# Kernel tuning notes

Hardware: AMD Instinct MI355X
Metric: run time of the kernel (lower is better)

The kernel has to match this reference:

```python
import jax, jax.numpy as jnp
import numpy as np

B, LQ, LK = 4, 1024, 2048
DQ, DK, DV, D = 1024, 512, 512, 1024
H = 16
HD = D // H
EPS = 1e-5


def setup_inputs() -> dict:
    key = jax.random.key(0)
    ks = jax.random.split(key, 12)
    s = lambda fan: 1.0 / np.sqrt(fan)
    return {
        "query": jax.random.normal(ks[0], (B, LQ, DQ), jnp.float32),
        "key": jax.random.normal(ks[1], (B, LK, DK), jnp.float32),
        "value": jax.random.normal(ks[2], (B, LK, DV), jnp.float32),
        "key_padding_mask": jnp.ones((B, LK), jnp.int32),
        "Wq": jax.random.normal(ks[3], (DQ, D), jnp.float32) * s(DQ),
        "bq": jnp.zeros((D,), jnp.float32),
        "Wk": jax.random.normal(ks[4], (DK, D), jnp.float32) * s(DK),
        "bk": jnp.zeros((D,), jnp.float32),
        "Wv": jax.random.normal(ks[5], (DV, D), jnp.float32) * s(DV),
        "bv": jnp.zeros((D,), jnp.float32),
        "Wo": jax.random.normal(ks[6], (D, D), jnp.float32) * s(D),
        "bo": jnp.zeros((D,), jnp.float32),
        "ln_g": jnp.ones((D,), jnp.float32),
        "ln_b": jnp.zeros((D,), jnp.float32),
    }


def _layer_norm(x, g, b):
    mu = jnp.mean(x, axis=-1, keepdims=True)
    var = jnp.mean(jnp.square(x - mu), axis=-1, keepdims=True)
    return (x - mu) * jax.lax.rsqrt(var + EPS) * g + b


def reference(query, key, value, key_padding_mask, Wq, bq, Wk, bk, Wv, bv, Wo, bo, ln_g, ln_b):
    residual = query
    qn = _layer_norm(query, ln_g, ln_b)
    # projections -> [B, L, H, HD]
    q = (qn @ Wq + bq).reshape(B, LQ, H, HD)
    k = (key @ Wk + bk).reshape(B, LK, H, HD)
    v = (value @ Wv + bv).reshape(B, LK, H, HD)
    scale = HD ** -0.5
    # scores [B, H, Lq, Lk]
    scores = jnp.einsum("bqhd,bkhd->bhqk", q, k) * scale
    mask = (key_padding_mask != 0)[:, None, None, :]  # True = keep
    scores = jnp.where(mask, scores, -jnp.inf)
    attn = jax.nn.softmax(scores, axis=-1)
    # dropout is identity in eval mode
    ctx = jnp.einsum("bhqk,bkhd->bqhd", attn, v).reshape(B, LQ, D)
    out = ctx @ Wo + bo
    return out + residual
```

## Files before the change

### kernel.cpp

```cpp
#include <hip/hip_runtime.h>
#include <hip/hip_bf16.h>
#include <stdint.h>

#define Bn 4
#define LQ 1024
#define LK 2048
#define Dm 1024
#define Hn 16
#define HD 64

typedef __attribute__((ext_vector_type(4))) float f32x4;
typedef __attribute__((ext_vector_type(8))) short bf16x8;
typedef __attribute__((ext_vector_type(2))) uint32_t u32x2;

__device__ __forceinline__ ushort f2bf(float f) {
  union { float f; uint32_t u; } v; v.f = f;
  uint32_t r = v.u + 0x7FFF + ((v.u >> 16) & 1);
  return (ushort)(r >> 16);
}

__device__ __forceinline__ uint32_t cvt_pk_bf16(float lo, float hi) {
  uint32_t r;
  asm("v_cvt_pk_bf16_f32 %0, %1, %2" : "=v"(r) : "v"(lo), "v"(hi));
  return r;
}

__device__ __forceinline__ float exp2v(float x) {
  float r;
  asm("v_exp_f32 %0, %1" : "=v"(r) : "v"(x));
  return r;
}

__device__ __forceinline__ void gload16(const void* g, void* lds) {
  __builtin_amdgcn_global_load_lds(
      (const __attribute__((address_space(1))) void*)g,
      (__attribute__((address_space(3))) void*)lds, 16, 0, 0);
}

__device__ __forceinline__ void wait_vm0_barrier() {
  asm volatile("s_waitcnt vmcnt(0)" ::: "memory");
  __builtin_amdgcn_s_barrier();
}

__global__ __launch_bounds__(256) void transpose_cast_kernel(
    const float* __restrict__ W, ushort* __restrict__ Wt, int K, int N) {
  __shared__ float tile[64][65];
  int k0 = blockIdx.x * 64, n0 = blockIdx.y * 64;
  int tx = threadIdx.x & 63, ty = threadIdx.x >> 6;
#pragma unroll
  for (int i = 0; i < 16; ++i) {
    int r = ty + i * 4;
    tile[r][tx] = W[(size_t)(k0 + r) * N + n0 + tx];
  }
  __syncthreads();
#pragma unroll
  for (int i = 0; i < 16; ++i) {
    int r = ty + i * 4;
    Wt[(size_t)(n0 + r) * K + k0 + tx] = f2bf(tile[tx][r]);
  }
}

__global__ __launch_bounds__(256) void cast_bf16_kernel(
    const float4* __restrict__ in, ushort4* __restrict__ out, int n4) {
  int i = blockIdx.x * blockDim.x + threadIdx.x;
  int stride = gridDim.x * blockDim.x;
  for (; i < n4; i += stride) {
    float4 v = in[i];
    out[i] = make_ushort4(f2bf(v.x), f2bf(v.y), f2bf(v.z), f2bf(v.w));
  }
}

__global__ __launch_bounds__(256) void ln_kernel(
    const float* __restrict__ x, const float* __restrict__ g,
    const float* __restrict__ b, ushort* __restrict__ y) {
  int row = blockIdx.x;
  const float4* xr = (const float4*)(x + (size_t)row * 1024);
  float4 v = xr[threadIdx.x];
  float s1 = v.x + v.y + v.z + v.w;
  float s2 = v.x * v.x + v.y * v.y + v.z * v.z + v.w * v.w;
#pragma unroll
  for (int off = 32; off > 0; off >>= 1) {
    s1 += __shfl_down(s1, off);
    s2 += __shfl_down(s2, off);
  }
  __shared__ float r1[4], r2[4];
  int w = threadIdx.x >> 6, lane = threadIdx.x & 63;
  if (lane == 0) { r1[w] = s1; r2[w] = s2; }
  __syncthreads();
  s1 = r1[0] + r1[1] + r1[2] + r1[3];
  s2 = r2[0] + r2[1] + r2[2] + r2[3];
  float mu = s1 * (1.0f / 1024.0f);
  float var = s2 * (1.0f / 1024.0f) - mu * mu;
  float rstd = rsqrtf(var + 1e-5f);
  float4 gv = ((const float4*)g)[threadIdx.x];
  float4 bv = ((const float4*)b)[threadIdx.x];
  ushort4 o;
  o.x = f2bf((v.x - mu) * rstd * gv.x + bv.x);
  o.y = f2bf((v.y - mu) * rstd * gv.y + bv.y);
  o.z = f2bf((v.z - mu) * rstd * gv.z + bv.z);
  o.w = f2bf((v.w - mu) * rstd * gv.w + bv.w);
  ((ushort4*)(y + (size_t)row * 1024))[threadIdx.x] = o;
}

template <int EPI>
__global__ __launch_bounds__(512) void gemm_bt_kernel(
    const ushort* __restrict__ A, const ushort* __restrict__ Bt,
    const float* __restrict__ bias, void* __restrict__ Cout,
    const float* __restrict__ residual, int M, int N, int K, float osc) {
  __shared__ ushort As[2][128 * 64];
  __shared__ ushort Bs[2][128 * 64];
  const int t = threadIdx.x;
  const int lane = t & 63;
  const int w = t >> 6;
  const int wm = w >> 2, wn = w & 3;
  const int m0 = blockIdx.y * 128, n0 = blockIdx.x * 128;
  const int l15 = lane & 15, g = lane >> 4;

  f32x4 acc[4][2] = {};

  const int c0 = t, c1 = t + 512;
  const int r0 = c0 >> 3, x0 = ((c0 & 7) ^ (r0 & 7)) * 8;
  const int r1 = c1 >> 3, x1 = ((c1 & 7) ^ (r1 & 7)) * 8;
  const ushort* Ap0 = A + (size_t)(m0 + r0) * K + x0;
  const ushort* Ap1 = A + (size_t)(m0 + r1) * K + x1;
  const ushort* Bp0 = Bt + (size_t)(n0 + r0) * K + x0;
  const ushort* Bp1 = Bt + (size_t)(n0 + r1) * K + x1;

  auto stage = [&](int buf, int kt) {
    gload16(Ap0 + kt, (char*)As[buf] + c0 * 16);
    gload16(Ap1 + kt, (char*)As[buf] + c1 * 16);
    gload16(Bp0 + kt, (char*)Bs[buf] + c0 * 16);
    gload16(Bp1 + kt, (char*)Bs[buf] + c1 * 16);
  };

  stage(0, 0);
  wait_vm0_barrier();

  int cur = 0;
  for (int kt = 0; kt < K; kt += 64) {
    if (kt + 64 < K) stage(cur ^ 1, kt + 64);
    bf16x8 af[4][2], bfr[2][2];
#pragma unroll
    for (int m = 0; m < 4; ++m) {
      int row = wm * 64 + m * 16 + l15;
#pragma unroll
      for (int kc = 0; kc < 2; ++kc)
        af[m][kc] = *(const bf16x8*)(As[cur] + row * 64 + ((kc * 4 + g) ^ (row & 7)) * 8);
    }
#pragma unroll
    for (int n = 0; n < 2; ++n) {
      int row = wn * 32 + n * 16 + l15;
#pragma unroll
      for (int kc = 0; kc < 2; ++kc)
        bfr[n][kc] = *(const bf16x8*)(Bs[cur] + row * 64 + ((kc * 4 + g) ^ (row & 7)) * 8);
    }
#pragma unroll
    for (int m = 0; m < 4; ++m)
#pragma unroll
      for (int n = 0; n < 2; ++n)
#pragma unroll
        for (int kc = 0; kc < 2; ++kc)
          acc[m][n] = __builtin_amdgcn_mfma_f32_16x16x32_bf16(af[m][kc], bfr[n][kc], acc[m][n], 0, 0, 0);
    wait_vm0_barrier();
    cur ^= 1;
  }

  float bias_v[2];
#pragma unroll
  for (int n = 0; n < 2; ++n) bias_v[n] = bias[n0 + wn * 32 + n * 16 + l15];

#pragma unroll
  for (int m = 0; m < 4; ++m) {
#pragma unroll
    for (int n = 0; n < 2; ++n) {
      int col = n0 + wn * 32 + n * 16 + l15;
      if (EPI == 1) {
        int row_base = m0 + wm * 64 + m * 16 + g * 4;
        int bb = row_base >> 11;
        int key = row_base & 2047;
        int h = col >> 6, hd = col & 63;
        ushort4 pk;
        pk.x = f2bf(acc[m][n][0] + bias_v[n]);
        pk.y = f2bf(acc[m][n][1] + bias_v[n]);
        pk.z = f2bf(acc[m][n][2] + bias_v[n]);
        pk.w = f2bf(acc[m][n][3] + bias_v[n]);
        *(ushort4*)((ushort*)Cout + ((size_t)((bb * 16 + h) * 64 + hd)) * 2048 + key) = pk;
      } else {
#pragma unroll
        for (int j = 0; j < 4; ++j) {
          int row = m0 + wm * 64 + m * 16 + g * 4 + j;
          if (EPI == 0) {
            float v = (acc[m][n][j] + bias_v[n]) * osc;
            ((ushort*)Cout)[(size_t)row * N + col] = f2bf(v);
          } else {
            size_t idx = (size_t)row * N + col;
            ((float*)Cout)[idx] = acc[m][n][j] + bias_v[n] + residual[idx];
          }
        }
      }
    }
  }
}

__global__ __launch_bounds__(512) void attn_kernel(
    const ushort* __restrict__ Qb, const ushort* __restrict__ Kb,
    const ushort* __restrict__ Vt, const int* __restrict__ mask,
    ushort* __restrict__ ctx) {
  __shared__ float mbias[2048];
  __shared__ ushort Ks[2][64 * 64];
  __shared__ ushort Vs[2][64 * 64];
  __shared__ ushort Ps[8][16 * 64];

  const int t = threadIdx.x, lane = t & 63, w = t >> 6;
  const int l15 = lane & 15, g = lane >> 4, g4 = g * 4;
  int o = blockIdx.x;
  int logical = (o & 7) * 64 + (o >> 3);
  const int b = logical >> 7;
  const int h = (logical >> 3) & 15;
  const int q0 = (logical & 7) * 128;
  const int* maskp = mask + b * 2048;

  const int rA = t >> 3;
  const int xA = ((t & 7) ^ (rA & 7)) * 8;
  const ushort* kp = Kb + ((size_t)(b * 2048 + rA)) * 1024 + h * 64 + xA;
  const ushort* vp = Vt + ((size_t)((b * 16 + h) * 64 + rA)) * 2048 + xA;

  auto stageKV = [&](int buf) {
    gload16(kp, (char*)Ks[buf] + t * 16);
    gload16(vp, (char*)Vs[buf] + t * 16);
  };

  stageKV(0);
  for (int i = t; i < 2048; i += 512) mbias[i] = maskp[i] ? 0.0f : -1e30f;

  bf16x8 aq[2];
  {
    int qrow = q0 + w * 16 + l15;
    const ushort* qp = Qb + ((size_t)(b * 1024 + qrow)) * 1024 + h * 64;
    aq[0] = *(const bf16x8*)(qp + g * 8);
    aq[1] = *(const bf16x8*)(qp + 32 + g * 8);
  }

  f32x4 o_acc[4] = {};
  float m_run = -1e30f, l_run = 0.0f;

  wait_vm0_barrier();

  char* pw = (char*)Ps[w];
  const int swz = (l15 & 7) << 4;

  int cur = 0;
  for (int kt = 0; kt < 2048; kt += 64) {
    kp += 64 * 1024;
    vp += 64;
    if (kt + 64 < 2048) stageKV(cur ^ 1);

    f32x4 sacc[4] = {};
    __builtin_amdgcn_s_setprio(1);
#pragma unroll
    for (int n = 0; n < 4; ++n) {
      int key = n * 16 + l15;
#pragma unroll
      for (int kc = 0; kc < 2; ++kc) {
        int kb2 = (kc * 32 + g * 8) * 2;
        bf16x8 kf = *(const bf16x8*)((char*)Ks[cur] + key * 128 + (kb2 ^ ((key & 7) << 4)));
        sacc[n] = __builtin_amdgcn_mfma_f32_16x16x32_bf16(kf, aq[kc], sacc[n], 0, 0, 0);
      }
    }
    __builtin_amdgcn_s_setprio(0);

    float sv[4][4];
    float tm = -1e30f;
#pragma unroll
    for (int n = 0; n < 4; ++n) {
      float4 mb = *(const float4*)&mbias[kt + n * 16 + g4];
      sv[n][0] = sacc[n][0] + mb.x;
      sv[n][1] = sacc[n][1] + mb.y;
      sv[n][2] = sacc[n][2] + mb.z;
      sv[n][3] = sacc[n][3] + mb.w;
      tm = fmaxf(tm, fmaxf(fmaxf(sv[n][0], sv[n][1]), fmaxf(sv[n][2], sv[n][3])));
    }
    tm = fmaxf(tm, __shfl_xor(tm, 16));
    tm = fmaxf(tm, __shfl_xor(tm, 32));

    if (__any(tm - m_run > 11.5f)) {
      float mn = fmaxf(m_run, tm);
      float al = exp2v(m_run - mn);
      m_run = mn;
      l_run *= al;
      float ao[4];
#pragma unroll
      for (int j = 0; j < 4; ++j) ao[j] = __shfl(al, g4 + j);
#pragma unroll
      for (int df = 0; df < 4; ++df)
#pragma unroll
        for (int j = 0; j < 4; ++j) o_acc[df][j] *= ao[j];
    }

    float psum = 0.0f;
    u32x2 pk[4];
#pragma unroll
    for (int n = 0; n < 4; ++n) {
      float p0 = exp2v(sv[n][0] - m_run);
      float p1 = exp2v(sv[n][1] - m_run);
      float p2 = exp2v(sv[n][2] - m_run);
      float p3 = exp2v(sv[n][3] - m_run);
      psum += (p0 + p1) + (p2 + p3);
      pk[n][0] = cvt_pk_bf16(p0, p1);
      pk[n][1] = cvt_pk_bf16(p2, p3);
    }
    psum += __shfl_xor(psum, 16);
    psum += __shfl_xor(psum, 32);
    l_run += psum;

    char* prow = pw + l15 * 128;
#pragma unroll
    for (int n = 0; n < 4; ++n)
      *(u32x2*)(prow + ((n * 32 + g * 8) ^ swz)) = pk[n];

    __builtin_amdgcn_s_setprio(1);
#pragma unroll
    for (int kc = 0; kc < 2; ++kc) {
      int kb2 = (kc * 32 + g * 8) * 2;
      bf16x8 pa = *(const bf16x8*)(prow + ((kc * 64 + g * 16) ^ swz));
#pragma unroll
      for (int df = 0; df < 4; ++df) {
        int d = df * 16 + l15;
        bf16x8 bv = *(const bf16x8*)((char*)Vs[cur] + d * 128 + (kb2 ^ ((d & 7) << 4)));
        o_acc[df] = __builtin_amdgcn_mfma_f32_16x16x32_bf16(pa, bv, o_acc[df], 0, 0, 0);
      }
    }
    __builtin_amdgcn_s_setprio(0);

    wait_vm0_barrier();
    cur ^= 1;
  }

  float inv[4];
#pragma unroll
  for (int j = 0; j < 4; ++j) inv[j] = 1.0f / __shfl(l_run, g4 + j);
  int qrow_base = q0 + w * 16 + g4;
#pragma unroll
  for (int df = 0; df < 4; ++df) {
    int col = h * 64 + df * 16 + l15;
#pragma unroll
    for (int j = 0; j < 4; ++j) {
      int qrow = qrow_base + j;
      ctx[((size_t)(b * 1024 + qrow)) * 1024 + col] = f2bf(o_acc[df][j] * inv[j]);
    }
  }
}

extern "C" void kernel_launch(void* const* d_in, const int* in_sizes, int n_in,
                              void* d_out, int out_size, void* d_ws, size_t ws_size,
                              hipStream_t stream) {
  const float* query = (const float*)d_in[0];
  const float* key   = (const float*)d_in[1];
  const float* value = (const float*)d_in[2];
  const int*   mask  = (const int*)d_in[3];
  const float* Wq = (const float*)d_in[4];
  const float* bq = (const float*)d_in[5];
  const float* Wk = (const float*)d_in[6];
  const float* bk = (const float*)d_in[7];
  const float* Wv = (const float*)d_in[8];
  const float* bv = (const float*)d_in[9];
  const float* Wo = (const float*)d_in[10];
  const float* bo = (const float*)d_in[11];
  const float* ln_g = (const float*)d_in[12];
  const float* ln_b = (const float*)d_in[13];
  float* out = (float*)d_out;

  char* p = (char*)d_ws;
  auto alloc = [&](size_t elems) { ushort* r = (ushort*)p; p += elems * 2; return r; };
  ushort* WqT  = alloc((size_t)1024 * 1024);
  ushort* WkT  = alloc((size_t)1024 * 512);
  ushort* WvT  = alloc((size_t)1024 * 512);
  ushort* WoT  = alloc((size_t)1024 * 1024);
  ushort* qn   = alloc((size_t)4096 * 1024);
  ushort* keyb = alloc((size_t)8192 * 512);
  ushort* valb = alloc((size_t)8192 * 512);
  ushort* Qb   = alloc((size_t)4096 * 1024);
  ushort* Kb   = alloc((size_t)8192 * 1024);
  ushort* Vt   = alloc((size_t)8192 * 1024);
  ushort* ctx  = alloc((size_t)4096 * 1024);
  (void)ws_size; (void)in_sizes; (void)n_in; (void)out_size;

  const float QSCALE = 0.125f * 1.44269504f;

  dim3 blk(256);
  dim3 blk5(512);
  transpose_cast_kernel<<<dim3(16, 16), blk, 0, stream>>>(Wq, WqT, 1024, 1024);
  transpose_cast_kernel<<<dim3(8, 16),  blk, 0, stream>>>(Wk, WkT, 512, 1024);
  transpose_cast_kernel<<<dim3(8, 16),  blk, 0, stream>>>(Wv, WvT, 512, 1024);
  transpose_cast_kernel<<<dim3(16, 16), blk, 0, stream>>>(Wo, WoT, 1024, 1024);
  cast_bf16_kernel<<<dim3(1024), blk, 0, stream>>>((const float4*)key,   (ushort4*)keyb, (8192 * 512) / 4);
  cast_bf16_kernel<<<dim3(1024), blk, 0, stream>>>((const float4*)value, (ushort4*)valb, (8192 * 512) / 4);
  ln_kernel<<<dim3(4096), blk, 0, stream>>>(query, ln_g, ln_b, qn);

  gemm_bt_kernel<0><<<dim3(8, 32), blk5, 0, stream>>>(qn,   WqT, bq, Qb, nullptr, 4096, 1024, 1024, QSCALE);
  gemm_bt_kernel<0><<<dim3(8, 64), blk5, 0, stream>>>(keyb, WkT, bk, Kb, nullptr, 8192, 1024, 512, 1.0f);
  gemm_bt_kernel<1><<<dim3(8, 64), blk5, 0, stream>>>(valb, WvT, bv, Vt, nullptr, 8192, 1024, 512, 1.0f);

  attn_kernel<<<dim3(512), blk5, 0, stream>>>(Qb, Kb, Vt, mask, ctx);

  gemm_bt_kernel<2><<<dim3(8, 32), blk5, 0, stream>>>(ctx, WoT, bo, out, query, 4096, 1024, 1024, 1.0f);
}
```

Measured before the change: 163.3 us.

## Switch GEMM and attention to 32x32x16 MFMA with 4-wave blocks

Both the projection GEMMs and the attention kernel move from 16x16x32 to 32x32x16 bf16 MFMA tiles, with 256-thread blocks where each wave owns a 64x64 GEMM tile or 32 query rows. In attention, the P matrix now stays in registers and is rearranged with cross-half lane shuffles instead of going through an LDS round trip. The output is staged through LDS so ctx is written with 16-byte coalesced stores. The aim is fewer LDS reads per MFMA and less LDS traffic, at the cost of more accumulator registers per wave and fewer waves per block to hide latency.

```diff
diff --git a/kernel.cpp b/kernel.cpp
--- a/kernel.cpp
+++ b/kernel.cpp
@@ -10,8 +10,8 @@
 #define HD 64
 
 typedef __attribute__((ext_vector_type(4))) float f32x4;
+typedef __attribute__((ext_vector_type(16))) float f32x16;
 typedef __attribute__((ext_vector_type(8))) short bf16x8;
-typedef __attribute__((ext_vector_type(2))) uint32_t u32x2;
 
 __device__ __forceinline__ ushort f2bf(float f) {
   union { float f; uint32_t u; } v; v.f = f;
@@ -39,6 +39,11 @@
 
 __device__ __forceinline__ void wait_vm0_barrier() {
   asm volatile("s_waitcnt vmcnt(0)" ::: "memory");
+  __builtin_amdgcn_s_barrier();
+}
+
+__device__ __forceinline__ void wait_all_barrier() {
+  asm volatile("s_waitcnt vmcnt(0) lgkmcnt(0)" ::: "memory");
   __builtin_amdgcn_s_barrier();
 }
 
@@ -103,7 +108,7 @@
 }
 
 template <int EPI>
-__global__ __launch_bounds__(512) void gemm_bt_kernel(
+__global__ __launch_bounds__(256) void gemm_bt_kernel(
     const ushort* __restrict__ A, const ushort* __restrict__ Bt,
     const float* __restrict__ bias, void* __restrict__ Cout,
     const float* __restrict__ residual, int M, int N, int K, float osc) {
@@ -112,25 +117,28 @@
   const int t = threadIdx.x;
   const int lane = t & 63;
   const int w = t >> 6;
-  const int wm = w >> 2, wn = w & 3;
+  const int wm = w >> 1, wn = w & 1;
   const int m0 = blockIdx.y * 128, n0 = blockIdx.x * 128;
-  const int l15 = lane & 15, g = lane >> 4;
-
-  f32x4 acc[4][2] = {};
-
-  const int c0 = t, c1 = t + 512;
-  const int r0 = c0 >> 3, x0 = ((c0 & 7) ^ (r0 & 7)) * 8;
-  const int r1 = c1 >> 3, x1 = ((c1 & 7) ^ (r1 & 7)) * 8;
-  const ushort* Ap0 = A + (size_t)(m0 + r0) * K + x0;
-  const ushort* Ap1 = A + (size_t)(m0 + r1) * K + x1;
-  const ushort* Bp0 = Bt + (size_t)(n0 + r0) * K + x0;
-  const ushort* Bp1 = Bt + (size_t)(n0 + r1) * K + x1;
+  const int l31 = lane & 31, hl = lane >> 5;
+
+  f32x16 acc[2][2] = {};
+
+  const ushort* Ap[4];
+  const ushort* Bp[4];
+#pragma unroll
+  for (int i = 0; i < 4; ++i) {
+    int c = t + i * 256;
+    int r = c >> 3, x = ((c & 7) ^ (r & 7)) * 8;
+    Ap[i] = A + (size_t)(m0 + r) * K + x;
+    Bp[i] = Bt + (size_t)(n0 + r) * K + x;
+  }
 
   auto stage = [&](int buf, int kt) {
-    gload16(Ap0 + kt, (char*)As[buf] + c0 * 16);
-    gload16(Ap1 + kt, (char*)As[buf] + c1 * 16);
-    gload16(Bp0 + kt, (char*)Bs[buf] + c0 * 16);
-    gload16(Bp1 + kt, (char*)Bs[buf] + c1 * 16);
+#pragma unroll
+    for (int i = 0; i < 4; ++i) {
+      gload16(Ap[i] + kt, (char*)As[buf] + (t + i * 256) * 16);
+      gload16(Bp[i] + kt, (char*)Bs[buf] + (t + i * 256) * 16);
+    }
   };
 
   stage(0, 0);
@@ -139,62 +147,70 @@
   int cur = 0;
   for (int kt = 0; kt < K; kt += 64) {
     if (kt + 64 < K) stage(cur ^ 1, kt + 64);
-    bf16x8 af[4][2], bfr[2][2];
-#pragma unroll
-    for (int m = 0; m < 4; ++m) {
-      int row = wm * 64 + m * 16 + l15;
-#pragma unroll
-      for (int kc = 0; kc < 2; ++kc)
-        af[m][kc] = *(const bf16x8*)(As[cur] + row * 64 + ((kc * 4 + g) ^ (row & 7)) * 8);
+    bf16x8 af[2][4], bfr[2][4];
+#pragma unroll
+    for (int m = 0; m < 2; ++m) {
+      int row = wm * 64 + m * 32 + l31;
+      const char* ar = (const char*)As[cur] + row * 128;
+      int rs = row & 7;
+#pragma unroll
+      for (int kc = 0; kc < 4; ++kc)
+        af[m][kc] = *(const bf16x8*)(ar + ((kc * 2 + hl) ^ rs) * 16);
     }
 #pragma unroll
     for (int n = 0; n < 2; ++n) {
-      int row = wn * 32 + n * 16 + l15;
-#pragma unroll
-      for (int kc = 0; kc < 2; ++kc)
-        bfr[n][kc] = *(const bf16x8*)(Bs[cur] + row * 64 + ((kc * 4 + g) ^ (row & 7)) * 8);
-    }
-#pragma unroll
-    for (int m = 0; m < 4; ++m)
-#pragma unroll
-      for (int n = 0; n < 2; ++n)
-#pragma unroll
-        for (int kc = 0; kc < 2; ++kc)
-          acc[m][n] = __builtin_amdgcn_mfma_f32_16x16x32_bf16(af[m][kc], bfr[n][kc], acc[m][n], 0, 0, 0);
+      int row = wn * 64 + n * 32 + l31;
+      const char* br = (const char*)Bs[cur] + row * 128;
+      int rs = row & 7;
+#pragma unroll
+      for (int kc = 0; kc < 4; ++kc)
+        bfr[n][kc] = *(const bf16x8*)(br + ((kc * 2 + hl) ^ rs) * 16);
+    }
+#pragma unroll
+    for (int kc = 0; kc < 4; ++kc)
+#pragma unroll
+      for (int m = 0; m < 2; ++m)
+#pragma unroll
+        for (int n = 0; n < 2; ++n)
+          acc[m][n] = __builtin_amdgcn_mfma_f32_32x32x16_bf16(af[m][kc], bfr[n][kc], acc[m][n], 0, 0, 0);
     wait_vm0_barrier();
     cur ^= 1;
   }
 
   float bias_v[2];
 #pragma unroll
-  for (int n = 0; n < 2; ++n) bias_v[n] = bias[n0 + wn * 32 + n * 16 + l15];
-
-#pragma unroll
-  for (int m = 0; m < 4; ++m) {
+  for (int n = 0; n < 2; ++n) bias_v[n] = bias[n0 + wn * 64 + n * 32 + l31];
+
+#pragma unroll
+  for (int m = 0; m < 2; ++m) {
+    int rbase = m0 + wm * 64 + m * 32 + hl * 4;
 #pragma unroll
     for (int n = 0; n < 2; ++n) {
-      int col = n0 + wn * 32 + n * 16 + l15;
-      if (EPI == 1) {
-        int row_base = m0 + wm * 64 + m * 16 + g * 4;
-        int bb = row_base >> 11;
-        int key = row_base & 2047;
-        int h = col >> 6, hd = col & 63;
-        ushort4 pk;
-        pk.x = f2bf(acc[m][n][0] + bias_v[n]);
-        pk.y = f2bf(acc[m][n][1] + bias_v[n]);
-        pk.z = f2bf(acc[m][n][2] + bias_v[n]);
-        pk.w = f2bf(acc[m][n][3] + bias_v[n]);
-        *(ushort4*)((ushort*)Cout + ((size_t)((bb * 16 + h) * 64 + hd)) * 2048 + key) = pk;
-      } else {
-#pragma unroll
-        for (int j = 0; j < 4; ++j) {
-          int row = m0 + wm * 64 + m * 16 + g * 4 + j;
-          if (EPI == 0) {
-            float v = (acc[m][n][j] + bias_v[n]) * osc;
-            ((ushort*)Cout)[(size_t)row * N + col] = f2bf(v);
-          } else {
-            size_t idx = (size_t)row * N + col;
-            ((float*)Cout)[idx] = acc[m][n][j] + bias_v[n] + residual[idx];
+      int col = n0 + wn * 64 + n * 32 + l31;
+#pragma unroll
+      for (int rq = 0; rq < 4; ++rq) {
+        int row0 = rbase + rq * 8;
+        if (EPI == 1) {
+          int bb = row0 >> 11;
+          int key = row0 & 2047;
+          int h = col >> 6, hd = col & 63;
+          ushort4 pk;
+          pk.x = f2bf(acc[m][n][rq * 4 + 0] + bias_v[n]);
+          pk.y = f2bf(acc[m][n][rq * 4 + 1] + bias_v[n]);
+          pk.z = f2bf(acc[m][n][rq * 4 + 2] + bias_v[n]);
+          pk.w = f2bf(acc[m][n][rq * 4 + 3] + bias_v[n]);
+          *(ushort4*)((ushort*)Cout + ((size_t)((bb * 16 + h) * 64 + hd)) * 2048 + key) = pk;
+        } else {
+#pragma unroll
+          for (int j = 0; j < 4; ++j) {
+            int row = row0 + j;
+            if (EPI == 0) {
+              float v = (acc[m][n][rq * 4 + j] + bias_v[n]) * osc;
+              ((ushort*)Cout)[(size_t)row * N + col] = f2bf(v);
+            } else {
+              size_t idx = (size_t)row * N + col;
+              ((float*)Cout)[idx] = acc[m][n][rq * 4 + j] + bias_v[n] + residual[idx];
+            }
           }
         }
       }
@@ -202,85 +218,92 @@
   }
 }
 
-__global__ __launch_bounds__(512) void attn_kernel(
+__global__ __launch_bounds__(256) void attn_kernel(
     const ushort* __restrict__ Qb, const ushort* __restrict__ Kb,
     const ushort* __restrict__ Vt, const int* __restrict__ mask,
     ushort* __restrict__ ctx) {
   __shared__ float mbias[2048];
   __shared__ ushort Ks[2][64 * 64];
   __shared__ ushort Vs[2][64 * 64];
-  __shared__ ushort Ps[8][16 * 64];
+  __shared__ ushort obuf[4][32 * 64];
 
   const int t = threadIdx.x, lane = t & 63, w = t >> 6;
-  const int l15 = lane & 15, g = lane >> 4, g4 = g * 4;
+  const int l31 = lane & 31, hl = lane >> 5;
   int o = blockIdx.x;
   int logical = (o & 7) * 64 + (o >> 3);
   const int b = logical >> 7;
-  const int h = (logical >> 3) & 15;
+  const int hh = (logical >> 3) & 15;
   const int q0 = (logical & 7) * 128;
   const int* maskp = mask + b * 2048;
 
-  const int rA = t >> 3;
-  const int xA = ((t & 7) ^ (rA & 7)) * 8;
-  const ushort* kp = Kb + ((size_t)(b * 2048 + rA)) * 1024 + h * 64 + xA;
-  const ushort* vp = Vt + ((size_t)((b * 16 + h) * 64 + rA)) * 2048 + xA;
+  const int cA = t, cB = t + 256;
+  const int rA = cA >> 3, rB = cB >> 3;
+  const int xA = ((cA & 7) ^ (rA & 7)) * 8, xB = ((cB & 7) ^ (rB & 7)) * 8;
+  const ushort* kpA = Kb + ((size_t)(b * 2048 + rA)) * 1024 + hh * 64 + xA;
+  const ushort* kpB = Kb + ((size_t)(b * 2048 + rB)) * 1024 + hh * 64 + xB;
+  const ushort* vpA = Vt + ((size_t)((b * 16 + hh) * 64 + rA)) * 2048 + xA;
+  const ushort* vpB = Vt + ((size_t)((b * 16 + hh) * 64 + rB)) * 2048 + xB;
 
   auto stageKV = [&](int buf) {
-    gload16(kp, (char*)Ks[buf] + t * 16);
-    gload16(vp, (char*)Vs[buf] + t * 16);
+    gload16(kpA, (char*)Ks[buf] + cA * 16);
+    gload16(kpB, (char*)Ks[buf] + cB * 16);
+    gload16(vpA, (char*)Vs[buf] + cA * 16);
+    gload16(vpB, (char*)Vs[buf] + cB * 16);
   };
 
   stageKV(0);
-  for (int i = t; i < 2048; i += 512) mbias[i] = maskp[i] ? 0.0f : -1e30f;
-
-  bf16x8 aq[2];
+  for (int i = t; i < 2048; i += 256) mbias[i] = maskp[i] ? 0.0f : -1e30f;
+
+  bf16x8 qf[4];
   {
-    int qrow = q0 + w * 16 + l15;
-    const ushort* qp = Qb + ((size_t)(b * 1024 + qrow)) * 1024 + h * 64;
-    aq[0] = *(const bf16x8*)(qp + g * 8);
-    aq[1] = *(const bf16x8*)(qp + 32 + g * 8);
-  }
-
-  f32x4 o_acc[4] = {};
+    int qrow = q0 + w * 32 + l31;
+    const ushort* qp = Qb + ((size_t)(b * 1024 + qrow)) * 1024 + hh * 64 + hl * 8;
+    qf[0] = *(const bf16x8*)(qp);
+    qf[1] = *(const bf16x8*)(qp + 16);
+    qf[2] = *(const bf16x8*)(qp + 32);
+    qf[3] = *(const bf16x8*)(qp + 48);
+  }
+
+  f32x16 o_acc[2] = {};
   float m_run = -1e30f, l_run = 0.0f;
 
-  wait_vm0_barrier();
-
-  char* pw = (char*)Ps[w];
-  const int swz = (l15 & 7) << 4;
+  wait_all_barrier();
 
   int cur = 0;
   for (int kt = 0; kt < 2048; kt += 64) {
-    kp += 64 * 1024;
-    vp += 64;
+    kpA += 64 * 1024; kpB += 64 * 1024; vpA += 64; vpB += 64;
     if (kt + 64 < 2048) stageKV(cur ^ 1);
 
-    f32x4 sacc[4] = {};
+    f32x16 sacc[2] = {};
     __builtin_amdgcn_s_setprio(1);
 #pragma unroll
-    for (int n = 0; n < 4; ++n) {
-      int key = n * 16 + l15;
-#pragma unroll
-      for (int kc = 0; kc < 2; ++kc) {
-        int kb2 = (kc * 32 + g * 8) * 2;
-        bf16x8 kf = *(const bf16x8*)((char*)Ks[cur] + key * 128 + (kb2 ^ ((key & 7) << 4)));
-        sacc[n] = __builtin_amdgcn_mfma_f32_16x16x32_bf16(kf, aq[kc], sacc[n], 0, 0, 0);
+    for (int kb = 0; kb < 2; ++kb) {
+      int row = kb * 32 + l31;
+      const char* krow = (const char*)Ks[cur] + row * 128;
+      int rs = row & 7;
+#pragma unroll
+      for (int kc = 0; kc < 4; ++kc) {
+        bf16x8 kf = *(const bf16x8*)(krow + ((kc * 2 + hl) ^ rs) * 16);
+        sacc[kb] = __builtin_amdgcn_mfma_f32_32x32x16_bf16(kf, qf[kc], sacc[kb], 0, 0, 0);
       }
     }
     __builtin_amdgcn_s_setprio(0);
 
-    float sv[4][4];
+    float p[2][16];
     float tm = -1e30f;
 #pragma unroll
-    for (int n = 0; n < 4; ++n) {
-      float4 mb = *(const float4*)&mbias[kt + n * 16 + g4];
-      sv[n][0] = sacc[n][0] + mb.x;
-      sv[n][1] = sacc[n][1] + mb.y;
-      sv[n][2] = sacc[n][2] + mb.z;
-      sv[n][3] = sacc[n][3] + mb.w;
-      tm = fmaxf(tm, fmaxf(fmaxf(sv[n][0], sv[n][1]), fmaxf(sv[n][2], sv[n][3])));
-    }
-    tm = fmaxf(tm, __shfl_xor(tm, 16));
+    for (int kb = 0; kb < 2; ++kb)
+#pragma unroll
+      for (int rq = 0; rq < 4; ++rq) {
+        float4 mb = *(const float4*)&mbias[kt + kb * 32 + rq * 8 + hl * 4];
+        float v0 = sacc[kb][rq * 4 + 0] + mb.x;
+        float v1 = sacc[kb][rq * 4 + 1] + mb.y;
+        float v2 = sacc[kb][rq * 4 + 2] + mb.z;
+        float v3 = sacc[kb][rq * 4 + 3] + mb.w;
+        p[kb][rq * 4 + 0] = v0; p[kb][rq * 4 + 1] = v1;
+        p[kb][rq * 4 + 2] = v2; p[kb][rq * 4 + 3] = v3;
+        tm = fmaxf(tm, fmaxf(fmaxf(v0, v1), fmaxf(v2, v3)));
+      }
     tm = fmaxf(tm, __shfl_xor(tm, 32));
 
     if (__any(tm - m_run > 11.5f)) {
@@ -288,46 +311,46 @@
       float al = exp2v(m_run - mn);
       m_run = mn;
       l_run *= al;
-      float ao[4];
-#pragma unroll
-      for (int j = 0; j < 4; ++j) ao[j] = __shfl(al, g4 + j);
-#pragma unroll
-      for (int df = 0; df < 4; ++df)
-#pragma unroll
-        for (int j = 0; j < 4; ++j) o_acc[df][j] *= ao[j];
+#pragma unroll
+      for (int df = 0; df < 2; ++df)
+#pragma unroll
+        for (int r = 0; r < 16; ++r) o_acc[df][r] *= al;
     }
 
     float psum = 0.0f;
-    u32x2 pk[4];
-#pragma unroll
-    for (int n = 0; n < 4; ++n) {
-      float p0 = exp2v(sv[n][0] - m_run);
-      float p1 = exp2v(sv[n][1] - m_run);
-      float p2 = exp2v(sv[n][2] - m_run);
-      float p3 = exp2v(sv[n][3] - m_run);
-      psum += (p0 + p1) + (p2 + p3);
-      pk[n][0] = cvt_pk_bf16(p0, p1);
-      pk[n][1] = cvt_pk_bf16(p2, p3);
-    }
-    psum += __shfl_xor(psum, 16);
+    uint32_t cpk[2][8];
+#pragma unroll
+    for (int kb = 0; kb < 2; ++kb)
+#pragma unroll
+      for (int rr = 0; rr < 8; ++rr) {
+        float pa = exp2v(p[kb][2 * rr] - m_run);
+        float pb = exp2v(p[kb][2 * rr + 1] - m_run);
+        psum += pa + pb;
+        cpk[kb][rr] = cvt_pk_bf16(pa, pb);
+      }
     psum += __shfl_xor(psum, 32);
     l_run += psum;
 
-    char* prow = pw + l15 * 128;
-#pragma unroll
-    for (int n = 0; n < 4; ++n)
-      *(u32x2*)(prow + ((n * 32 + g * 8) ^ swz)) = pk[n];
-
     __builtin_amdgcn_s_setprio(1);
 #pragma unroll
-    for (int kc = 0; kc < 2; ++kc) {
-      int kb2 = (kc * 32 + g * 8) * 2;
-      bf16x8 pa = *(const bf16x8*)(prow + ((kc * 64 + g * 16) ^ swz));
-#pragma unroll
-      for (int df = 0; df < 4; ++df) {
-        int d = df * 16 + l15;
-        bf16x8 bv = *(const bf16x8*)((char*)Vs[cur] + d * 128 + (kb2 ^ ((d & 7) << 4)));
-        o_acc[df] = __builtin_amdgcn_mfma_f32_16x16x32_bf16(pa, bv, o_acc[df], 0, 0, 0);
+    for (int ks = 0; ks < 4; ++ks) {
+      const int kb = ks >> 1, ci = (ks & 1) * 4;
+      uint32_t send0 = hl ? cpk[kb][ci] : cpk[kb][ci + 2];
+      uint32_t send1 = hl ? cpk[kb][ci + 1] : cpk[kb][ci + 3];
+      uint32_t recv0 = (uint32_t)__shfl_xor((int)send0, 32);
+      uint32_t recv1 = (uint32_t)__shfl_xor((int)send1, 32);
+      uint32_t own0 = hl ? cpk[kb][ci + 2] : cpk[kb][ci];
+      uint32_t own1 = hl ? cpk[kb][ci + 3] : cpk[kb][ci + 1];
+      union { uint32_t u[4]; bf16x8 v; } pb_;
+      pb_.u[0] = hl ? recv0 : own0;
+      pb_.u[1] = hl ? recv1 : own1;
+      pb_.u[2] = hl ? own0 : recv0;
+      pb_.u[3] = hl ? own1 : recv1;
+#pragma unroll
+      for (int df = 0; df < 2; ++df) {
+        int row = df * 32 + l31;
+        bf16x8 vf = *(const bf16x8*)((const char*)Vs[cur] + row * 128 + ((ks * 2 + hl) ^ (row & 7)) * 16);
+        o_acc[df] = __builtin_amdgcn_mfma_f32_32x32x16_bf16(vf, pb_.v, o_acc[df], 0, 0, 0);
       }
     }
     __builtin_amdgcn_s_setprio(0);
@@ -336,18 +359,27 @@
     cur ^= 1;
   }
 
-  float inv[4];
-#pragma unroll
-  for (int j = 0; j < 4; ++j) inv[j] = 1.0f / __shfl(l_run, g4 + j);
-  int qrow_base = q0 + w * 16 + g4;
-#pragma unroll
-  for (int df = 0; df < 4; ++df) {
-    int col = h * 64 + df * 16 + l15;
-#pragma unroll
-    for (int j = 0; j < 4; ++j) {
-      int qrow = qrow_base + j;
-      ctx[((size_t)(b * 1024 + qrow)) * 1024 + col] = f2bf(o_acc[df][j] * inv[j]);
-    }
+  float inv = 1.0f / l_run;
+  char* ob = (char*)obuf[w];
+#pragma unroll
+  for (int df = 0; df < 2; ++df)
+#pragma unroll
+    for (int rq = 0; rq < 4; ++rq) {
+      ushort4 pk;
+      pk.x = f2bf(o_acc[df][rq * 4 + 0] * inv);
+      pk.y = f2bf(o_acc[df][rq * 4 + 1] * inv);
+      pk.z = f2bf(o_acc[df][rq * 4 + 2] * inv);
+      pk.w = f2bf(o_acc[df][rq * 4 + 3] * inv);
+      *(ushort4*)(ob + l31 * 128 + (((df * 4 + rq) ^ (l31 & 7)) * 16) + hl * 8) = pk;
+    }
+  asm volatile("s_waitcnt lgkmcnt(0)" ::: "memory");
+#pragma unroll
+  for (int i = 0; i < 4; ++i) {
+    int q = (lane >> 3) + i * 8;
+    int ch = lane & 7;
+    uint4 v = *(const uint4*)(ob + q * 128 + ((ch ^ (q & 7)) * 16));
+    int qrow = q0 + w * 32 + q;
+    *(uint4*)(ctx + ((size_t)(b * 1024 + qrow)) * 1024 + hh * 64 + ch * 8) = v;
   }
 }
 
@@ -388,7 +420,6 @@
   const float QSCALE = 0.125f * 1.44269504f;
 
   dim3 blk(256);
-  dim3 blk5(512);
   transpose_cast_kernel<<<dim3(16, 16), blk, 0, stream>>>(Wq, WqT, 1024, 1024);
   transpose_cast_kernel<<<dim3(8, 16),  blk, 0, stream>>>(Wk, WkT, 512, 1024);
   transpose_cast_kernel<<<dim3(8, 16),  blk, 0, stream>>>(Wv, WvT, 512, 1024);
@@ -397,11 +428,11 @@
   cast_bf16_kernel<<<dim3(1024), blk, 0, stream>>>((const float4*)value, (ushort4*)valb, (8192 * 512) / 4);
   ln_kernel<<<dim3(4096), blk, 0, stream>>>(query, ln_g, ln_b, qn);
 
-  gemm_bt_kernel<0><<<dim3(8, 32), blk5, 0, stream>>>(qn,   WqT, bq, Qb, nullptr, 4096, 1024, 1024, QSCALE);
-  gemm_bt_kernel<0><<<dim3(8, 64), blk5, 0, stream>>>(keyb, WkT, bk, Kb, nullptr, 8192, 1024, 512, 1.0f);
-  gemm_bt_kernel<1><<<dim3(8, 64), blk5, 0, stream>>>(valb, WvT, bv, Vt, nullptr, 8192, 1024, 512, 1.0f);
-
-  attn_kernel<<<dim3(512), blk5, 0, stream>>>(Qb, Kb, Vt, mask, ctx);
-
-  gemm_bt_kernel<2><<<dim3(8, 32), blk5, 0, stream>>>(ctx, WoT, bo, out, query, 4096, 1024, 1024, 1.0f);
-}
+  gemm_bt_kernel<0><<<dim3(8, 32), blk, 0, stream>>>(qn,   WqT, bq, Qb, nullptr, 4096, 1024, 1024, QSCALE);
+  gemm_bt_kernel<0><<<dim3(8, 64), blk, 0, stream>>>(keyb, WkT, bk, Kb, nullptr, 8192, 1024, 512, 1.0f);
+  gemm_bt_kernel<1><<<dim3(8, 64), blk, 0, stream>>>(valb, WvT, bv, Vt, nullptr, 8192, 1024, 512, 1.0f);
+
+  attn_kernel<<<dim3(512), blk, 0, stream>>>(Qb, Kb, Vt, mask, ctx);
+
+  gemm_bt_kernel<2><<<dim3(8, 32), blk, 0, stream>>>(ctx, WoT, bo, out, query, 4096, 1024, 1024, 1.0f);
+}
```

After: 176.1 us. 7.8% more time.
